# Performance work log

Hardware: AMD Instinct MI355X
Metric: run time of the kernel (lower is better)

## Reference

```python
import jax, jax.numpy as jnp
import numpy as np


def setup_inputs() -> dict:
    key = jax.random.key(0)
    kq, kk, kv = jax.random.split(key, 3)
    B, H, S, D = 1, 16, 4096, 64
    Q = jax.random.normal(kq, (B, H, S, D), dtype=jnp.float32)
    K = jax.random.normal(kk, (B, H, S, D), dtype=jnp.float32)
    V = jax.random.normal(kv, (B, H, S, D), dtype=jnp.float32)
    return {"Q": Q, "K": K, "V": V}


def reference(Q, K, V):
    # scores: [B, H, len_q, len_k], scaled by sqrt(dim_k)
    dim_k = K.shape[-1]
    scale = 1.0 / jnp.sqrt(jnp.asarray(dim_k, dtype=Q.dtype))
    scores = jnp.einsum("bhqd,bhkd->bhqk", Q, K) * scale
    attention = jax.nn.softmax(scores, axis=-1)
    context = jnp.einsum("bhqk,bhkd->bhqd", attention, V)
    return context
```

## Files before the change

kernel.cpp:

```cpp
#include <hip/hip_runtime.h>
#include <hip/hip_bf16.h>

typedef short bf16x8 __attribute__((ext_vector_type(8)));
typedef __bf16 bfv8  __attribute__((ext_vector_type(8)));
typedef __bf16 bfv4  __attribute__((ext_vector_type(4)));
typedef float f32x4  __attribute__((ext_vector_type(4)));

#define S_LEN 4096
#define DDIM  64
#define KVB   32
#define QBLK  128
#define NHEAD 16
#define THR   7.0f
#define VOFFB 4096
#define BUFSZ 9216

#define MFMA(a, b, c) __builtin_amdgcn_mfma_f32_16x16x32_bf16((a), (b), (c), 0, 0, 0)

static __device__ __forceinline__ float exp2v(float x) {
    return __builtin_amdgcn_exp2f(x);
}

static __device__ __forceinline__ int4 cvt8(float4 a, float4 b) {
    bfv8 r;
    r[0] = (__bf16)a.x; r[1] = (__bf16)a.y; r[2] = (__bf16)a.z; r[3] = (__bf16)a.w;
    r[4] = (__bf16)b.x; r[5] = (__bf16)b.y; r[6] = (__bf16)b.z; r[7] = (__bf16)b.w;
    return __builtin_bit_cast(int4, r);
}
static __device__ __forceinline__ int2 cvt4(f32x4 a) {
    bfv4 r;
    r[0] = (__bf16)a[0]; r[1] = (__bf16)a[1]; r[2] = (__bf16)a[2]; r[3] = (__bf16)a[3];
    return __builtin_bit_cast(int2, r);
}

static __device__ __forceinline__ bf16x8 ldfrag(const unsigned char* base, int row, int doff) {
    int addr = (row * 128 + doff * 2) ^ ((row & 7) << 4);
    return *reinterpret_cast<const bf16x8*>(base + addr);
}

static __device__ __forceinline__ void stage(unsigned char* base, int kdst, int vdst,
                                             int4 kv, int4 vv) {
    *reinterpret_cast<int4*>(base + kdst)         = kv;
    *reinterpret_cast<int4*>(base + VOFFB + vdst) = vv;
}

static __device__ __forceinline__ bf16x8 softmax_pb(f32x4 s0, f32x4 s1, float& m,
                                                    f32x4 acc[4], f32x4& lacc) {
    float mx = fmaxf(fmaxf(fmaxf(s0[0], s0[1]), s0[2]),
                     fmaxf(fmaxf(s0[3], s1[0]),
                           fmaxf(s1[1], fmaxf(s1[2], s1[3]))));
    if (!__all(mx <= m + THR)) {
        float pm = fmaxf(mx, __shfl_xor(mx, 16));
        pm = fmaxf(pm, __shfl_xor(pm, 32));
        float mn = fmaxf(m, pm);
        float al = exp2v(m - mn);
        #pragma unroll
        for (int dk = 0; dk < 4; ++dk)
            #pragma unroll
            for (int j = 0; j < 4; ++j) acc[dk][j] *= al;
        #pragma unroll
        for (int j = 0; j < 4; ++j) lacc[j] *= al;
        m = mn;
    }
    bfv8 r;
    #pragma unroll
    for (int j = 0; j < 4; ++j) {
        r[2 * j]     = (__bf16)exp2v(s0[j] - m);
        r[2 * j + 1] = (__bf16)exp2v(s1[j] - m);
    }
    return __builtin_bit_cast(bf16x8, r);
}

__global__ __launch_bounds__(256) void prep(
    const float* __restrict__ Kg, const float* __restrict__ Vg,
    unsigned short* __restrict__ wsKT, unsigned short* __restrict__ wsVT)
{
    const int h  = blockIdx.y;
    const int kt = blockIdx.x;
    const int t  = threadIdx.x;
    const int srow = t >> 3;
    const int sd   = (t & 7) * 8;
    const size_t src = (((size_t)h * S_LEN) + (size_t)kt * 32 + srow) * DDIM + sd;

    {
        float4 a = *reinterpret_cast<const float4*>(Kg + src);
        float4 b = *reinterpret_cast<const float4*>(Kg + src + 4);
        const int swK = (srow * 128 + sd * 2) ^ ((srow & 7) << 4);
        *reinterpret_cast<int4*>(reinterpret_cast<char*>(wsKT)
            + ((size_t)(h * 128 + kt) << 12) + swK) = cvt8(a, b);
    }

    __shared__ __align__(16) unsigned short vt[32][68];
    {
        float4 a = *reinterpret_cast<const float4*>(Vg + src);
        float4 b = *reinterpret_cast<const float4*>(Vg + src + 4);
        int4 w = cvt8(a, b);
        int2 lo = {w.x, w.y}, hi = {w.z, w.w};
        *reinterpret_cast<int2*>(&vt[srow][sd])     = lo;
        *reinterpret_cast<int2*>(&vt[srow][sd + 4]) = hi;
    }
    __syncthreads();
    {
        const int d  = t >> 2;
        const int p0 = (t & 3) * 8;
        unsigned short out[8];
        #pragma unroll
        for (int i = 0; i < 8; ++i) {
            int p   = p0 + i;
            int key = 4 * (p >> 3) + ((p & 7) >> 1) + 16 * (p & 1);
            out[i] = vt[key][d];
        }
        *reinterpret_cast<int4*>(wsVT + ((size_t)(h * 128 + kt) * 2048) + d * 32 + p0)
            = *reinterpret_cast<const int4*>(out);
    }
}

template <int KSPLIT>
__global__ __launch_bounds__(256, 4) void attn_fwd(
    const float* __restrict__ Qg, const unsigned short* __restrict__ wsKT,
    const unsigned short* __restrict__ wsVT, float* __restrict__ Og,
    unsigned short* __restrict__ wsO, float* __restrict__ wsML)
{
    const int h    = blockIdx.y;
    const int qb   = blockIdx.x;
    const int ks   = (KSPLIT > 1) ? blockIdx.z : 0;
    const int kt0  = ks * (128 / KSPLIT);
    const int NT   = 128 / KSPLIT;
    const int tid  = threadIdx.x;
    const int lane = tid & 63;
    const int wv   = tid >> 6;
    const int g    = lane >> 4;
    const int r16  = lane & 15;

    __shared__ __align__(16) unsigned char lds[2 * BUFSZ];

    const float QSC = 0.125f * 1.44269504088896f;
    const int qrow0 = qb * QBLK + wv * 32 + r16;
    bf16x8 qf0[2], qf1[2];
    {
        const float* qp0 = Qg + ((size_t)h * S_LEN + qrow0) * DDIM;
        const float* qp1 = qp0 + 16 * DDIM;
        #pragma unroll
        for (int c = 0; c < 2; ++c) {
            float4 x = *reinterpret_cast<const float4*>(qp0 + 32 * c + 8 * g);
            float4 y = *reinterpret_cast<const float4*>(qp0 + 32 * c + 8 * g + 4);
            float4 xs = {x.x * QSC, x.y * QSC, x.z * QSC, x.w * QSC};
            float4 ys = {y.x * QSC, y.y * QSC, y.z * QSC, y.w * QSC};
            qf0[c] = __builtin_bit_cast(bf16x8, cvt8(xs, ys));
            x = *reinterpret_cast<const float4*>(qp1 + 32 * c + 8 * g);
            y = *reinterpret_cast<const float4*>(qp1 + 32 * c + 8 * g + 4);
            xs = {x.x * QSC, x.y * QSC, x.z * QSC, x.w * QSC};
            ys = {y.x * QSC, y.y * QSC, y.z * QSC, y.w * QSC};
            qf1[c] = __builtin_bit_cast(bf16x8, cvt8(xs, ys));
        }
    }

    bf16x8 ones;
    #pragma unroll
    for (int e = 0; e < 8; ++e) ones[e] = (short)0x3F80;

    const int kdst = tid * 16;
    const int vdst = (tid >> 2) * 80 + (tid & 3) * 16;
    const unsigned short* ktp = wsKT + ((size_t)(h * 128 + kt0) * 2048) + tid * 8;
    const unsigned short* vtp = wsVT + ((size_t)(h * 128 + kt0) * 2048)
                              + (tid >> 2) * 32 + (tid & 3) * 8;

    int4 kv = *reinterpret_cast<const int4*>(ktp);
    int4 vv = *reinterpret_cast<const int4*>(vtp);
    stage(lds, kdst, vdst, kv, vv);
    ktp += 2048; vtp += 2048;
    kv = *reinterpret_cast<const int4*>(ktp);
    vv = *reinterpret_cast<const int4*>(vtp);
    __syncthreads();

    const f32x4 z0 = {0.f, 0.f, 0.f, 0.f};
    f32x4 accA[4] = {z0, z0, z0, z0};
    f32x4 accB[4] = {z0, z0, z0, z0};
    f32x4 laccA = z0, laccB = z0;
    float m0 = -INFINITY, m1 = -INFINITY;

    int c = 0;
    for (int kt = 0; kt < NT; ++kt) {
        const unsigned char* Klds = lds + c * BUFSZ;
        const unsigned char* Vlds = Klds + VOFFB;

        if (kt + 1 < NT) {
            stage(lds + (c ^ 1) * BUFSZ, kdst, vdst, kv, vv);
            if (kt + 2 < NT) {
                ktp += 2048; vtp += 2048;
                kv = *reinterpret_cast<const int4*>(ktp);
                vv = *reinterpret_cast<const int4*>(vtp);
            }
        }

        bf16x8 vf[4];
        {
            const unsigned char* vbase = Vlds + r16 * 80 + 16 * g;
            #pragma unroll
            for (int dk = 0; dk < 4; ++dk)
                vf[dk] = *reinterpret_cast<const bf16x8*>(vbase + dk * 1280);
        }

        f32x4 sA0 = z0, sA1 = z0, sB0 = z0, sB1 = z0;
        #pragma unroll
        for (int cc = 0; cc < 2; ++cc) {
            bf16x8 k0 = ldfrag(Klds, r16,      32 * cc + 8 * g);
            bf16x8 k1 = ldfrag(Klds, 16 + r16, 32 * cc + 8 * g);
            sA0 = MFMA(k0, qf0[cc], sA0);
            sA1 = MFMA(k1, qf0[cc], sA1);
            sB0 = MFMA(k0, qf1[cc], sB0);
            sB1 = MFMA(k1, qf1[cc], sB1);
        }

        bf16x8 pbA = softmax_pb(sA0, sA1, m0, accA, laccA);
        bf16x8 pbB = softmax_pb(sB0, sB1, m1, accB, laccB);

        laccA = MFMA(ones, pbA, laccA);
        #pragma unroll
        for (int dk = 0; dk < 4; ++dk) accA[dk] = MFMA(vf[dk], pbA, accA[dk]);
        laccB = MFMA(ones, pbB, laccB);
        #pragma unroll
        for (int dk = 0; dk < 4; ++dk) accB[dk] = MFMA(vf[dk], pbB, accB[dk]);

        __syncthreads();
        c ^= 1;
    }

    if (KSPLIT == 1) {
        float inv0 = 1.0f / laccA[0];
        float* op = Og + ((size_t)h * S_LEN + qrow0) * DDIM;
        #pragma unroll
        for (int dk = 0; dk < 4; ++dk) {
            float4 o = {accA[dk][0] * inv0, accA[dk][1] * inv0,
                        accA[dk][2] * inv0, accA[dk][3] * inv0};
            *reinterpret_cast<float4*>(op + 16 * dk + 4 * g) = o;
        }
        float inv1 = 1.0f / laccB[0];
        op += 16 * DDIM;
        #pragma unroll
        for (int dk = 0; dk < 4; ++dk) {
            float4 o = {accB[dk][0] * inv1, accB[dk][1] * inv1,
                        accB[dk][2] * inv1, accB[dk][3] * inv1};
            *reinterpret_cast<float4*>(op + 16 * dk + 4 * g) = o;
        }
    } else {
        const size_t R0 = (size_t)h * S_LEN + qrow0;
        unsigned short* o0 = wsO + ((size_t)ks * (NHEAD * S_LEN) + R0) * DDIM;
        #pragma unroll
        for (int dk = 0; dk < 4; ++dk)
            *reinterpret_cast<int2*>(o0 + 16 * dk + 4 * g) = cvt4(accA[dk]);
        o0 += 16 * DDIM;
        #pragma unroll
        for (int dk = 0; dk < 4; ++dk)
            *reinterpret_cast<int2*>(o0 + 16 * dk + 4 * g) = cvt4(accB[dk]);
        if (g == 0) {
            float2 v0 = {m0, laccA[0]};
            float2 v1 = {m1, laccB[0]};
            *reinterpret_cast<float2*>(wsML + ((size_t)ks * (NHEAD * S_LEN) + R0) * 2)      = v0;
            *reinterpret_cast<float2*>(wsML + ((size_t)ks * (NHEAD * S_LEN) + R0 + 16) * 2) = v1;
        }
    }
}

template <int NS>
__global__ __launch_bounds__(256) void combineN(
    const unsigned short* __restrict__ wsO, const float* __restrict__ wsML,
    float* __restrict__ Og)
{
    const int NR = NHEAD * S_LEN;
    int t  = blockIdx.x * 256 + threadIdx.x;
    int R  = t >> 4;
    int d4 = (t & 15) * 4;
    float2 ml[NS];
    float m = -INFINITY;
    #pragma unroll
    for (int s = 0; s < NS; ++s) {
        ml[s] = *reinterpret_cast<const float2*>(wsML + ((size_t)s * NR + R) * 2);
        m = fmaxf(m, ml[s].x);
    }
    float a[NS], den = 0.f;
    #pragma unroll
    for (int s = 0; s < NS; ++s) { a[s] = exp2v(ml[s].x - m); den += a[s] * ml[s].y; }
    float inv = 1.0f / den;
    float4 o = {0.f, 0.f, 0.f, 0.f};
    #pragma unroll
    for (int s = 0; s < NS; ++s) {
        bfv4 ob = __builtin_bit_cast(bfv4,
            *reinterpret_cast<const int2*>(wsO + ((size_t)s * NR + R) * DDIM + d4));
        float w = a[s] * inv;
        o.x += w * (float)ob[0]; o.y += w * (float)ob[1];
        o.z += w * (float)ob[2]; o.w += w * (float)ob[3];
    }
    *reinterpret_cast<float4*>(Og + (size_t)R * DDIM + d4) = o;
}

extern "C" void kernel_launch(void* const* d_in, const int* in_sizes, int n_in,
                              void* d_out, int out_size, void* d_ws, size_t ws_size,
                              hipStream_t stream) {
    const float* Q = (const float*)d_in[0];
    const float* K = (const float*)d_in[1];
    const float* V = (const float*)d_in[2];
    float* O = (float*)d_out;

    const size_t nKT = (size_t)NHEAD * 128 * 2048;
    const size_t nVT = (size_t)NHEAD * 128 * 2048;
    const size_t nOrow = (size_t)NHEAD * S_LEN * DDIM;
    const size_t nMLrow = (size_t)NHEAD * S_LEN * 2;
    const size_t baseB  = (nKT + nVT) * 2;
    const size_t perSplitB = nOrow * 2 + nMLrow * 4;
    const size_t need2 = baseB + 2 * perSplitB;

    unsigned short* wsKT = (unsigned short*)d_ws;
    unsigned short* wsVT = wsKT + nKT;
    unsigned short* wsO  = wsVT + nVT;

    prep<<<dim3(128, NHEAD), dim3(256, 1, 1), 0, stream>>>(K, V, wsKT, wsVT);

    if (ws_size >= need2) {
        float* wsML = (float*)(wsO + 2 * nOrow);
        dim3 grid(S_LEN / QBLK, NHEAD, 2);
        attn_fwd<2><<<grid, dim3(256, 1, 1), 0, stream>>>(Q, wsKT, wsVT, O, wsO, wsML);
        int nthr = NHEAD * S_LEN * (DDIM / 4);
        combineN<2><<<dim3(nthr / 256), dim3(256, 1, 1), 0, stream>>>(wsO, wsML, O);
    } else {
        dim3 grid(S_LEN / QBLK, NHEAD, 1);
        attn_fwd<1><<<grid, dim3(256, 1, 1), 0, stream>>>(Q, wsKT, wsVT, O, nullptr, nullptr);
    }
}
```

Before: 101.9 us.

## Process two KV tiles per barrier with quad-buffered LDS staging

Each loop iteration now handles two 32-key KV tiles. The shared-memory ring grows from two buffers to four, and the next pair is prefetched into registers while the current pair is computed. This halves the number of __syncthreads barriers and gives each prefetch more compute to hide behind. The cost is twice the LDS and more live registers, and launch bounds drop from 4 to 3 blocks per SM, which lowers occupancy.

```diff
diff --git a/kernel.cpp b/kernel.cpp
--- a/kernel.cpp
+++ b/kernel.cpp
@@ -116,7 +116,7 @@
 }
 
 template <int KSPLIT>
-__global__ __launch_bounds__(256, 4) void attn_fwd(
+__global__ __launch_bounds__(256, 3) void attn_fwd(
     const float* __restrict__ Qg, const unsigned short* __restrict__ wsKT,
     const unsigned short* __restrict__ wsVT, float* __restrict__ Og,
     unsigned short* __restrict__ wsO, float* __restrict__ wsML)
@@ -126,13 +126,14 @@
     const int ks   = (KSPLIT > 1) ? blockIdx.z : 0;
     const int kt0  = ks * (128 / KSPLIT);
     const int NT   = 128 / KSPLIT;
+    const int NP   = NT / 2;
     const int tid  = threadIdx.x;
     const int lane = tid & 63;
     const int wv   = tid >> 6;
     const int g    = lane >> 4;
     const int r16  = lane & 15;
 
-    __shared__ __align__(16) unsigned char lds[2 * BUFSZ];
+    __shared__ __align__(16) unsigned char lds[4 * BUFSZ];
 
     const float QSC = 0.125f * 1.44269504088896f;
     const int qrow0 = qb * QBLK + wv * 32 + r16;
@@ -165,12 +166,17 @@
     const unsigned short* vtp = wsVT + ((size_t)(h * 128 + kt0) * 2048)
                               + (tid >> 2) * 32 + (tid & 3) * 8;
 
-    int4 kv = *reinterpret_cast<const int4*>(ktp);
-    int4 vv = *reinterpret_cast<const int4*>(vtp);
-    stage(lds, kdst, vdst, kv, vv);
-    ktp += 2048; vtp += 2048;
-    kv = *reinterpret_cast<const int4*>(ktp);
-    vv = *reinterpret_cast<const int4*>(vtp);
+    int4 kvA = *reinterpret_cast<const int4*>(ktp);
+    int4 vvA = *reinterpret_cast<const int4*>(vtp);
+    int4 kvB = *reinterpret_cast<const int4*>(ktp + 2048);
+    int4 vvB = *reinterpret_cast<const int4*>(vtp + 2048);
+    stage(lds,         kdst, vdst, kvA, vvA);
+    stage(lds + BUFSZ, kdst, vdst, kvB, vvB);
+    ktp += 4096; vtp += 4096;
+    kvA = *reinterpret_cast<const int4*>(ktp);
+    vvA = *reinterpret_cast<const int4*>(vtp);
+    kvB = *reinterpret_cast<const int4*>(ktp + 2048);
+    vvB = *reinterpret_cast<const int4*>(vtp + 2048);
     __syncthreads();
 
     const f32x4 z0 = {0.f, 0.f, 0.f, 0.f};
@@ -179,51 +185,57 @@
     f32x4 laccA = z0, laccB = z0;
     float m0 = -INFINITY, m1 = -INFINITY;
 
-    int c = 0;
-    for (int kt = 0; kt < NT; ++kt) {
-        const unsigned char* Klds = lds + c * BUFSZ;
-        const unsigned char* Vlds = Klds + VOFFB;
-
-        if (kt + 1 < NT) {
-            stage(lds + (c ^ 1) * BUFSZ, kdst, vdst, kv, vv);
-            if (kt + 2 < NT) {
-                ktp += 2048; vtp += 2048;
-                kv = *reinterpret_cast<const int4*>(ktp);
-                vv = *reinterpret_cast<const int4*>(vtp);
+    for (int p = 0; p < NP; ++p) {
+        if (p + 1 < NP) {
+            const int ns = ((p & 1) ^ 1) * 2;
+            stage(lds + ns * BUFSZ,       kdst, vdst, kvA, vvA);
+            stage(lds + (ns + 1) * BUFSZ, kdst, vdst, kvB, vvB);
+            if (p + 2 < NP) {
+                ktp += 4096; vtp += 4096;
+                kvA = *reinterpret_cast<const int4*>(ktp);
+                vvA = *reinterpret_cast<const int4*>(vtp);
+                kvB = *reinterpret_cast<const int4*>(ktp + 2048);
+                vvB = *reinterpret_cast<const int4*>(vtp + 2048);
             }
         }
 
-        bf16x8 vf[4];
-        {
-            const unsigned char* vbase = Vlds + r16 * 80 + 16 * g;
+        const int cs = (p & 1) * 2;
+        #pragma unroll
+        for (int u = 0; u < 2; ++u) {
+            const unsigned char* Klds = lds + (cs + u) * BUFSZ;
+            const unsigned char* Vlds = Klds + VOFFB;
+
+            bf16x8 vf[4];
+            {
+                const unsigned char* vbase = Vlds + r16 * 80 + 16 * g;
+                #pragma unroll
+                for (int dk = 0; dk < 4; ++dk)
+                    vf[dk] = *reinterpret_cast<const bf16x8*>(vbase + dk * 1280);
+            }
+
+            f32x4 sA0 = z0, sA1 = z0, sB0 = z0, sB1 = z0;
             #pragma unroll
-            for (int dk = 0; dk < 4; ++dk)
-                vf[dk] = *reinterpret_cast<const bf16x8*>(vbase + dk * 1280);
-        }
-
-        f32x4 sA0 = z0, sA1 = z0, sB0 = z0, sB1 = z0;
-        #pragma unroll
-        for (int cc = 0; cc < 2; ++cc) {
-            bf16x8 k0 = ldfrag(Klds, r16,      32 * cc + 8 * g);
-            bf16x8 k1 = ldfrag(Klds, 16 + r16, 32 * cc + 8 * g);
-            sA0 = MFMA(k0, qf0[cc], sA0);
-            sA1 = MFMA(k1, qf0[cc], sA1);
-            sB0 = MFMA(k0, qf1[cc], sB0);
-            sB1 = MFMA(k1, qf1[cc], sB1);
-        }
-
-        bf16x8 pbA = softmax_pb(sA0, sA1, m0, accA, laccA);
-        bf16x8 pbB = softmax_pb(sB0, sB1, m1, accB, laccB);
-
-        laccA = MFMA(ones, pbA, laccA);
-        #pragma unroll
-        for (int dk = 0; dk < 4; ++dk) accA[dk] = MFMA(vf[dk], pbA, accA[dk]);
-        laccB = MFMA(ones, pbB, laccB);
-        #pragma unroll
-        for (int dk = 0; dk < 4; ++dk) accB[dk] = MFMA(vf[dk], pbB, accB[dk]);
+            for (int cc = 0; cc < 2; ++cc) {
+                bf16x8 k0 = ldfrag(Klds, r16,      32 * cc + 8 * g);
+                bf16x8 k1 = ldfrag(Klds, 16 + r16, 32 * cc + 8 * g);
+                sA0 = MFMA(k0, qf0[cc], sA0);
+                sA1 = MFMA(k1, qf0[cc], sA1);
+                sB0 = MFMA(k0, qf1[cc], sB0);
+                sB1 = MFMA(k1, qf1[cc], sB1);
+            }
+
+            bf16x8 pbA = softmax_pb(sA0, sA1, m0, accA, laccA);
+            bf16x8 pbB = softmax_pb(sB0, sB1, m1, accB, laccB);
+
+            laccA = MFMA(ones, pbA, laccA);
+            #pragma unroll
+            for (int dk = 0; dk < 4; ++dk) accA[dk] = MFMA(vf[dk], pbA, accA[dk]);
+            laccB = MFMA(ones, pbB, laccB);
+            #pragma unroll
+            for (int dk = 0; dk < 4; ++dk) accB[dk] = MFMA(vf[dk], pbB, accB[dk]);
+        }
 
         __syncthreads();
-        c ^= 1;
     }
 
     if (KSPLIT == 1) {
```

After: 102.4 us. No clear change (+0.5%).

## Fold running max subtraction into QK MFMA accumulator init and add setprio

Applied to the files above, without the earlier changes.

The score MFMAs now start from a -m accumulator instead of zero, so the subtraction of the running max is done inside the matrix multiply and the exp2 step needs no per-element subtract. The rescale branch shifts the scores and updates m in place. Initial m becomes 0, not -inf, so the lazy rescale triggers only when scores exceed the threshold. The change also adds s_setprio around the MFMA blocks and lowers the launch-bounds minimum blocks from 4 to 3, which may allow more registers per thread at the cost of occupancy.

```diff
diff --git a/kernel.cpp b/kernel.cpp
--- a/kernel.cpp
+++ b/kernel.cpp
@@ -45,28 +45,31 @@
 }
 
 static __device__ __forceinline__ bf16x8 softmax_pb(f32x4 s0, f32x4 s1, float& m,
-                                                    f32x4 acc[4], f32x4& lacc) {
+                                                    f32x4& nmv, f32x4 acc[4],
+                                                    f32x4& lacc) {
     float mx = fmaxf(fmaxf(fmaxf(s0[0], s0[1]), s0[2]),
                      fmaxf(fmaxf(s0[3], s1[0]),
                            fmaxf(s1[1], fmaxf(s1[2], s1[3]))));
-    if (!__all(mx <= m + THR)) {
+    if (!__all(mx <= THR)) {
         float pm = fmaxf(mx, __shfl_xor(mx, 16));
         pm = fmaxf(pm, __shfl_xor(pm, 32));
-        float mn = fmaxf(m, pm);
-        float al = exp2v(m - mn);
+        pm = fmaxf(pm, 0.f);
+        float al = exp2v(-pm);
         #pragma unroll
         for (int dk = 0; dk < 4; ++dk)
             #pragma unroll
             for (int j = 0; j < 4; ++j) acc[dk][j] *= al;
         #pragma unroll
         for (int j = 0; j < 4; ++j) lacc[j] *= al;
-        m = mn;
+        m += pm;
+        #pragma unroll
+        for (int j = 0; j < 4; ++j) { s0[j] -= pm; s1[j] -= pm; nmv[j] = -m; }
     }
     bfv8 r;
     #pragma unroll
     for (int j = 0; j < 4; ++j) {
-        r[2 * j]     = (__bf16)exp2v(s0[j] - m);
-        r[2 * j + 1] = (__bf16)exp2v(s1[j] - m);
+        r[2 * j]     = (__bf16)exp2v(s0[j]);
+        r[2 * j + 1] = (__bf16)exp2v(s1[j]);
     }
     return __builtin_bit_cast(bf16x8, r);
 }
@@ -116,7 +119,7 @@
 }
 
 template <int KSPLIT>
-__global__ __launch_bounds__(256, 4) void attn_fwd(
+__global__ __launch_bounds__(256, 3) void attn_fwd(
     const float* __restrict__ Qg, const unsigned short* __restrict__ wsKT,
     const unsigned short* __restrict__ wsVT, float* __restrict__ Og,
     unsigned short* __restrict__ wsO, float* __restrict__ wsML)
@@ -177,7 +180,8 @@
     f32x4 accA[4] = {z0, z0, z0, z0};
     f32x4 accB[4] = {z0, z0, z0, z0};
     f32x4 laccA = z0, laccB = z0;
-    float m0 = -INFINITY, m1 = -INFINITY;
+    f32x4 nm0v = z0, nm1v = z0;
+    float m0 = 0.f, m1 = 0.f;
 
     int c = 0;
     for (int kt = 0; kt < NT; ++kt) {
@@ -201,26 +205,32 @@
                 vf[dk] = *reinterpret_cast<const bf16x8*>(vbase + dk * 1280);
         }
 
-        f32x4 sA0 = z0, sA1 = z0, sB0 = z0, sB1 = z0;
-        #pragma unroll
-        for (int cc = 0; cc < 2; ++cc) {
-            bf16x8 k0 = ldfrag(Klds, r16,      32 * cc + 8 * g);
-            bf16x8 k1 = ldfrag(Klds, 16 + r16, 32 * cc + 8 * g);
-            sA0 = MFMA(k0, qf0[cc], sA0);
-            sA1 = MFMA(k1, qf0[cc], sA1);
-            sB0 = MFMA(k0, qf1[cc], sB0);
-            sB1 = MFMA(k1, qf1[cc], sB1);
-        }
-
-        bf16x8 pbA = softmax_pb(sA0, sA1, m0, accA, laccA);
-        bf16x8 pbB = softmax_pb(sB0, sB1, m1, accB, laccB);
-
+        bf16x8 k00 = ldfrag(Klds, r16,      8 * g);
+        bf16x8 k10 = ldfrag(Klds, 16 + r16, 8 * g);
+        bf16x8 k01 = ldfrag(Klds, r16,      32 + 8 * g);
+        bf16x8 k11 = ldfrag(Klds, 16 + r16, 32 + 8 * g);
+        __builtin_amdgcn_s_setprio(1);
+        f32x4 sA0 = MFMA(k00, qf0[0], nm0v);
+        f32x4 sA1 = MFMA(k10, qf0[0], nm0v);
+        f32x4 sB0 = MFMA(k00, qf1[0], nm1v);
+        f32x4 sB1 = MFMA(k10, qf1[0], nm1v);
+        sA0 = MFMA(k01, qf0[1], sA0);
+        sA1 = MFMA(k11, qf0[1], sA1);
+        sB0 = MFMA(k01, qf1[1], sB0);
+        sB1 = MFMA(k11, qf1[1], sB1);
+        __builtin_amdgcn_s_setprio(0);
+
+        bf16x8 pbA = softmax_pb(sA0, sA1, m0, nm0v, accA, laccA);
+        bf16x8 pbB = softmax_pb(sB0, sB1, m1, nm1v, accB, laccB);
+
+        __builtin_amdgcn_s_setprio(1);
         laccA = MFMA(ones, pbA, laccA);
         #pragma unroll
         for (int dk = 0; dk < 4; ++dk) accA[dk] = MFMA(vf[dk], pbA, accA[dk]);
         laccB = MFMA(ones, pbB, laccB);
         #pragma unroll
         for (int dk = 0; dk < 4; ++dk) accB[dk] = MFMA(vf[dk], pbB, accB[dk]);
+        __builtin_amdgcn_s_setprio(0);
 
         __syncthreads();
         c ^= 1;
```

Result: no change. 103.4 us (+1.4%).
